# Kernel optimization log

Hardware: AMD Instinct MI355X
Metric: run time of the kernel (lower is better)

Reference implementation:

```python
import jax, jax.numpy as jnp
import numpy as np
from jax import lax

HEADS = 8
HEAD_C = 16  # attention_channels // heads = 128 // 8


def setup_inputs() -> dict:
    key = jax.random.key(0)
    ks = jax.random.split(key, 16)
    N, I, H, W = 8, 128, 36, 36
    R, C, A, O = 128, 128, 128, 128  # recurrent, common, attention, out channels
    s = lambda *sh: 0.05
    inp = {
        'x': jax.random.normal(ks[0], (N, I, H, W), jnp.float32),
        # input 1x1 conv (Accumulate of single Conv, bias init 0)
        'w_in': jax.random.normal(ks[1], (R, I), jnp.float32) * 0.05,
        'b_in': jnp.zeros((R,), jnp.float32),
        # 3x3 conv on cat([x, h]) -> common channels
        'w_conv': jax.random.normal(ks[2], (C, 2 * R, 3, 3), jnp.float32) * 0.05,
        'b_conv': jnp.zeros((C,), jnp.float32),
        # q/k/v 1x1 projections (no bias)
        'wq': jax.random.normal(ks[3], (A, C), jnp.float32) * 0.05,
        'wk': jax.random.normal(ks[4], (A, C), jnp.float32) * 0.05,
        'wv': jax.random.normal(ks[5], (A, C), jnp.float32) * 0.05,
        # gate 1x1 projections on cat([z, a]) (C + A inputs)
        'w_i': jax.random.normal(ks[6], (R, C + A), jnp.float32) * 0.05,
        'b_i': jnp.full((R,), -1.0, jnp.float32),  # init_input
        'w_f': jax.random.normal(ks[7], (R, C + A), jnp.float32) * 0.05,
        'b_f': jnp.full((R,), 1.0, jnp.float32),   # init_forget
        'w_g': jax.random.normal(ks[8], (R, C + A), jnp.float32) * 0.05,
        'b_g': jnp.zeros((R,), jnp.float32),
        'w_o': jax.random.normal(ks[9], (R, C + A), jnp.float32) * 0.05,
        'b_o': jnp.zeros((R,), jnp.float32),
        # output 1x1 conv
        'w_out': jax.random.normal(ks[10], (O, R), jnp.float32) * 0.05,
        'b_out': jnp.zeros((O,), jnp.float32),
    }
    return inp


def _conv1x1(w, x, b=None):
    y = jnp.einsum('oi,nihw->nohw', w, x)
    if b is not None:
        y = y + b[None, :, None, None]
    return y


def reference(x, w_in, b_in, w_conv, b_conv, wq, wk, wv,
              w_i, b_i, w_f, b_f, w_g, b_g, w_o, b_o, w_out, b_out):
    # first timestep: past is empty -> h = c = 0
    xt = jnp.tanh(_conv1x1(w_in, x, b_in))          # [N, R, H, W]
    h0 = jnp.zeros_like(xt)
    c0 = jnp.zeros_like(xt)
    xh = jnp.concatenate([xt, h0], axis=1)          # groups=1 -> plain concat
    z = lax.conv_general_dilated(xh, w_conv, (1, 1), 'SAME') + b_conv[None, :, None, None]
    N, C, H, W = z.shape
    HW = H * W
    q = _conv1x1(wq, z).reshape(N, HEADS, HEAD_C, HW)
    k = _conv1x1(wk, z).reshape(N, HEADS, HEAD_C, HW)
    v = _conv1x1(wv, z).reshape(N, HEADS, HEAD_C, HW)
    # spatial attention over H*W tokens per head
    w_attn = jax.nn.softmax(jnp.einsum('nhcq,nhcd->nhqd', q, k), axis=-1)  # [N,heads,HW,HW]
    a = jnp.einsum('nhcd,nhqd->nhcq', v, w_attn).reshape(N, -1, H, W)      # [N,A,H,W]
    za = jnp.concatenate([z, a], axis=1)
    i = jax.nn.sigmoid(_conv1x1(w_i, za, b_i))
    f = jax.nn.sigmoid(_conv1x1(w_f, za, b_f))
    g = jnp.tanh(_conv1x1(w_g, za, b_g))
    o = jax.nn.sigmoid(_conv1x1(w_o, za, b_o))
    c = f * c0 + i * g
    h = o * jnp.tanh(c)  # dropout p=0 -> identity
    return _conv1x1(w_out, h, b_out)
```

## Files before the change

### kernel.cpp

```cpp
#include <hip/hip_runtime.h>
#include <hip/hip_bf16.h>
#include <math.h>

typedef __hip_bfloat16 bf16;
typedef __attribute__((ext_vector_type(8))) short frag8;
typedef __attribute__((ext_vector_type(4))) float f32x4;
typedef __attribute__((ext_vector_type(16))) float f32x16;
typedef __attribute__((ext_vector_type(2))) unsigned int u32x2;
typedef __attribute__((ext_vector_type(4))) unsigned int u32x4;

#define HW  1296
#define CH  128
#define TT  1327104

__device__ __forceinline__ float b2f(bf16 v) { return __bfloat162float(v); }
__device__ __forceinline__ float bits2f(unsigned short u) {
    return __uint_as_float(((unsigned)u) << 16);
}
__device__ __forceinline__ float frcp(float x) { return __builtin_amdgcn_rcpf(x); }
__device__ __forceinline__ float fsigm(float x) { return frcp(1.0f + __expf(-x)); }
__device__ __forceinline__ float ftanh(float x) {
    float xc = fminf(15.0f, fmaxf(-15.0f, x));
    float e = __expf(2.0f * xc);
    return (e - 1.0f) * frcp(e + 1.0f);
}
__device__ __forceinline__ int packrh(float a, float b) {
    unsigned ua = __float_as_uint(a) + 0x8000u;
    unsigned ub = __float_as_uint(b) + 0x8000u;
    return (int)__builtin_amdgcn_perm(ub, ua, 0x07060302);
}
__device__ __forceinline__ int2 pack4(float a, float b, float c, float d) {
    int2 r; r.x = packrh(a, b); r.y = packrh(c, d); return r;
}
__device__ __forceinline__ unsigned cvtpk(float a, float b) {
    unsigned r;
    asm("v_cvt_pk_bf16_f32 %0, %1, %2" : "=v"(r) : "v"(a), "v"(b));
    return r;
}

__device__ __forceinline__ int detect_f32(const void* w) {
    const short4* p = (const short4*)w;
    short4 v = p[threadIdx.x & 63];
    int bad = 0;
    #pragma unroll
    for (int j = 0; j < 4; ++j) {
        float f = bits2f(((const unsigned short*)&v)[j]);
        if (!(fabsf(f) <= 100.0f)) bad = 1;
    }
    return __any(bad) ? 1 : 0;
}

__global__ __launch_bounds__(256) void k_prep(
    const void* w_in, const void* w_conv, const void* wq, const void* wk, const void* wv,
    const void* w_i, const void* w_g, const void* w_o, const void* w_out,
    const void* b_in, const void* b_conv, const void* b_i, const void* b_g,
    const void* b_o, const void* b_out,
    bf16* __restrict__ Wdst, float* __restrict__ Bdst)
{
    int idx = blockIdx.x * 256 + threadIdx.x;
    const int f = detect_f32(w_in);
    if (idx < 327680) {
        const void* src; int si;
        if (idx < 16384)       { src = w_in; si = idx; }
        else if (idx < 163840) { int j = idx - 16384; int tap = j >> 14, rem = j & 16383;
                                 int o = rem >> 7, r = rem & 127;
                                 src = w_conv; si = o * 2304 + r * 9 + tap; }
        else if (idx < 212992) { int j = idx - 163840; int o = j >> 7, i = j & 127;
                                 int ws_ = o >> 7;
                                 src = ws_ == 0 ? wq : ws_ == 1 ? wk : wv;
                                 si = (o & 127) * 128 + i; }
        else if (idx < 311296) { int j = idx - 212992; int g = j >> 15, rem = j & 32767;
                                 int o = rem >> 8, k = rem & 255;
                                 src = g == 0 ? w_i : g == 1 ? w_g : w_o; si = o * 256 + k; }
        else                   { int j = idx - 311296; int o = j >> 7, i = j & 127;
                                 src = w_out; si = o * 128 + i; }
        float v = f ? ((const float*)src)[si] : b2f(((const bf16*)src)[si]);
        if (idx >= 163840 && idx < 180224) v *= 1.4426950408889634f;
        Wdst[idx] = __float2bfloat16(v);
    } else if (idx < 327680 + 768) {
        int j = idx - 327680; int b = j >> 7, e = j & 127;
        const void* src = b == 0 ? b_in : b == 1 ? b_conv : b == 2 ? b_i
                        : b == 3 ? b_g : b == 4 ? b_o : b_out;
        Bdst[j] = f ? ((const float*)src)[e] : b2f(((const bf16*)src)[e]);
    }
}

__global__ __launch_bounds__(256) void k_inm(const void* __restrict__ x,
                                             const void* __restrict__ wraw,
                                             const bf16* __restrict__ Wm,
                                             const float* __restrict__ bias,
                                             bf16* __restrict__ XT) {
    __shared__ short Xl[32][132];
    const int tid = threadIdx.x, wave = tid >> 6, lane = tid & 63;
    const int quad = lane >> 4, l16 = lane & 15;
    const int n = blockIdx.x;
    const int pbase = blockIdx.y * 32;
    const int obase = blockIdx.z * 32 + (wave & 1) * 16;
    const int pstrip = (wave >> 1) * 16;
    const int f = detect_f32(wraw);

    frag8 WF[4];
    #pragma unroll
    for (int kc = 0; kc < 4; ++kc)
        WF[kc] = *(const frag8*)&Wm[(obase + l16) * CH + kc * 32 + quad * 8];

    #pragma unroll
    for (int rep = 0; rep < 4; ++rep) {
        int u = tid + rep * 256;
        int i = u >> 3;
        int p4 = (u & 7) * 4;
        int p = pbase + p4;
        short4 s = {0, 0, 0, 0};
        if (p < HW) {
            size_t gi = (size_t)n * CH * HW + (size_t)i * HW + p;
            if (f) {
                float4 fv = *(const float4*)((const float*)x + gi);
                int2 pk = pack4(fv.x, fv.y, fv.z, fv.w);
                s = *(short4*)&pk;
            } else {
                s = *(const short4*)((const bf16*)x + gi);
            }
        }
        Xl[p4 + 0][i] = s.x; Xl[p4 + 1][i] = s.y;
        Xl[p4 + 2][i] = s.z; Xl[p4 + 3][i] = s.w;
    }
    __syncthreads();

    const int pl = pstrip + l16;
    f32x4 acc = {0.f, 0.f, 0.f, 0.f};
    #pragma unroll
    for (int kc = 0; kc < 4; ++kc) {
        int k = kc * 32 + quad * 8;
        short4 b0 = *(const short4*)&Xl[pl][k];
        short4 b1 = *(const short4*)&Xl[pl][k + 4];
        frag8 bf = {b0.x, b0.y, b0.z, b0.w, b1.x, b1.y, b1.z, b1.w};
        acc = __builtin_amdgcn_mfma_f32_16x16x32_bf16(WF[kc], bf, acc, 0, 0, 0);
    }

    int p = pbase + pstrip + l16;
    if (p < HW) {
        int og = obase + quad * 4;
        int2 pk = pack4(ftanh(acc[0] + bias[og + 0]), ftanh(acc[1] + bias[og + 1]),
                        ftanh(acc[2] + bias[og + 2]), ftanh(acc[3] + bias[og + 3]));
        *(int2*)((short*)XT + ((size_t)n * HW + p) * CH + og) = pk;
    }
}

__global__ __launch_bounds__(512) void k_cq(
    const bf16* __restrict__ XT, const bf16* __restrict__ Wc,
    const float* __restrict__ bc, const bf16* __restrict__ Wqkv,
    bf16* __restrict__ Zb, bf16* __restrict__ Qb, bf16* __restrict__ Kb,
    bf16* __restrict__ Vb)
{
    __shared__ short Zl[32][136];
    const int tid = threadIdx.x, w = tid >> 6, lane = tid & 63;
    const int quad = lane >> 4, l16 = lane & 15;
    const int n = blockIdx.x;
    const int pbase = blockIdx.y * 32;
    const bf16* actn = XT + (size_t)n * HW * CH;

    const int obase = w * 16;
    const int p1 = pbase + l16, p2 = pbase + 16 + l16;
    const bool p1ok = p1 < HW, p2ok = p2 < HW;
    const int h1 = p1 / 36, w1 = p1 - h1 * 36;
    const int h2 = p2 / 36, w2 = p2 - h2 * 36;

    frag8 zf = {0, 0, 0, 0, 0, 0, 0, 0};
    f32x4 acc[2];
    acc[0] = (f32x4){0.f, 0.f, 0.f, 0.f};
    acc[1] = (f32x4){0.f, 0.f, 0.f, 0.f};

    frag8 A1[2][4], A2[2][4], WT[2][4];

    #define LOADTAP(TAP, BUF)                                                        \
    {                                                                                \
        const int dy = (TAP) / 3 - 1, dx = (TAP) - ((TAP) / 3) * 3 - 1;              \
        const bool ok1 = p1ok && (unsigned)(h1 + dy) < 36u && (unsigned)(w1 + dx) < 36u; \
        const bool ok2 = p2ok && (unsigned)(h2 + dy) < 36u && (unsigned)(w2 + dx) < 36u; \
        const int sh = dy * 36 + dx;                                                 \
        const bf16* a1 = actn + (size_t)(p1 + sh) * CH + quad * 8;                   \
        const bf16* a2 = actn + (size_t)(p2 + sh) * CH + quad * 8;                   \
        const bf16* wp = Wc + (TAP) * 16384 + (obase + l16) * CH + quad * 8;         \
        _Pragma("unroll")                                                            \
        for (int kc = 0; kc < 4; ++kc) {                                             \
            A1[BUF][kc] = ok1 ? *(const frag8*)&a1[kc * 32] : zf;                    \
            A2[BUF][kc] = ok2 ? *(const frag8*)&a2[kc * 32] : zf;                    \
            WT[BUF][kc] = *(const frag8*)&wp[kc * 32];                               \
        }                                                                            \
    }

    LOADTAP(0, 0);
    #pragma unroll
    for (int tap = 0; tap < 9; ++tap) {
        const int cur = tap & 1;
        if (tap < 8) LOADTAP(tap + 1, cur ^ 1);
        #pragma unroll
        for (int kc = 0; kc < 4; ++kc) {
            acc[0] = __builtin_amdgcn_mfma_f32_16x16x32_bf16(WT[cur][kc], A1[cur][kc], acc[0], 0, 0, 0);
            acc[1] = __builtin_amdgcn_mfma_f32_16x16x32_bf16(WT[cur][kc], A2[cur][kc], acc[1], 0, 0, 0);
        }
    }
    #undef LOADTAP

    const int og = obase + quad * 4;
    #pragma unroll
    for (int pt = 0; pt < 2; ++pt) {
        int p = pbase + pt * 16 + l16;
        int2 pk = pack4(acc[pt][0] + bc[og + 0], acc[pt][1] + bc[og + 1],
                        acc[pt][2] + bc[og + 2], acc[pt][3] + bc[og + 3]);
        *(int2*)&Zl[pt * 16 + l16][og] = pk;
        if (p < HW)
            *(int2*)((short*)Zb + ((size_t)n * HW + p) * CH + og) = pk;
    }
    __syncthreads();

    for (int ot = w; ot < 12; ot += 8) {
        const bool vt = (ot >= 8);
        const int ob = ot * 32;
        frag8 B1[4], B2[4], W0a[4], W1a[4];
        #pragma unroll
        for (int kc = 0; kc < 4; ++kc) {
            int ko = kc * 32 + quad * 8;
            B1[kc]  = *(const frag8*)&Zl[l16][ko];
            B2[kc]  = *(const frag8*)&Zl[16 + l16][ko];
            W0a[kc] = *(const frag8*)&Wqkv[(size_t)(ob + l16) * CH + ko];
            W1a[kc] = *(const frag8*)&Wqkv[(size_t)(ob + 16 + l16) * CH + ko];
        }

        f32x4 qacc[2][2];
        #pragma unroll
        for (int of = 0; of < 2; ++of) {
            qacc[of][0] = (f32x4){0.f, 0.f, 0.f, 0.f};
            qacc[of][1] = (f32x4){0.f, 0.f, 0.f, 0.f};
        }
        #pragma unroll
        for (int kc = 0; kc < 4; ++kc) {
            if (vt) {
                qacc[0][0] = __builtin_amdgcn_mfma_f32_16x16x32_bf16(B1[kc], W0a[kc], qacc[0][0], 0, 0, 0);
                qacc[0][1] = __builtin_amdgcn_mfma_f32_16x16x32_bf16(B2[kc], W0a[kc], qacc[0][1], 0, 0, 0);
                qacc[1][0] = __builtin_amdgcn_mfma_f32_16x16x32_bf16(B1[kc], W1a[kc], qacc[1][0], 0, 0, 0);
                qacc[1][1] = __builtin_amdgcn_mfma_f32_16x16x32_bf16(B2[kc], W1a[kc], qacc[1][1], 0, 0, 0);
            } else {
                qacc[0][0] = __builtin_amdgcn_mfma_f32_16x16x32_bf16(W0a[kc], B1[kc], qacc[0][0], 0, 0, 0);
                qacc[0][1] = __builtin_amdgcn_mfma_f32_16x16x32_bf16(W0a[kc], B2[kc], qacc[0][1], 0, 0, 0);
                qacc[1][0] = __builtin_amdgcn_mfma_f32_16x16x32_bf16(W1a[kc], B1[kc], qacc[1][0], 0, 0, 0);
                qacc[1][1] = __builtin_amdgcn_mfma_f32_16x16x32_bf16(W1a[kc], B2[kc], qacc[1][1], 0, 0, 0);
            }
        }

        if (vt) {
            #pragma unroll
            for (int of = 0; of < 2; ++of) {
                int ov = ob + of * 16 - 256 + l16;
                #pragma unroll
                for (int pt = 0; pt < 2; ++pt) {
                    int p4 = pbase + pt * 16 + quad * 4;
                    if (p4 >= HW) continue;
                    int2 pk = pack4(qacc[of][pt][0], qacc[of][pt][1], qacc[of][pt][2], qacc[of][pt][3]);
                    *(int2*)((short*)Vb + ((size_t)n * CH + ov) * HW + p4) = pk;
                }
            }
        } else {
            #pragma unroll
            for (int of = 0; of < 2; ++of) {
                int ogq = ob + of * 16 + quad * 4;
                int which = ogq >> 7, ol = ogq & 127;
                bf16* dst = which == 0 ? Qb : Kb;
                #pragma unroll
                for (int pt = 0; pt < 2; ++pt) {
                    int p = pbase + pt * 16 + l16;
                    if (p >= HW) continue;
                    size_t di = (((size_t)n * 8 + (ol >> 4)) * HW + p) * 16 + (ol & 15);
                    int2 pk = pack4(qacc[of][pt][0], qacc[of][pt][1], qacc[of][pt][2], qacc[of][pt][3]);
                    *(int2*)((short*)dst + di) = pk;
                }
            }
        }
    }
}

__global__ __launch_bounds__(256) void k_cell(
    const bf16* __restrict__ Zb, const bf16* __restrict__ Ab,
    const bf16* __restrict__ Wg, const float* __restrict__ bg,
    const bf16* __restrict__ Wo, const float* __restrict__ bo,
    void* __restrict__ out, const void* __restrict__ wraw)
{
    __shared__ short Hl[16][136];
    const int tid = threadIdx.x, w = tid >> 6, lane = tid & 63;
    const int quad = lane >> 4, l16 = lane & 15;
    const int n = blockIdx.x;
    const int pbase = blockIdx.y * 16;
    const int f32f = detect_f32(wraw);
    const bf16* zn = Zb + (size_t)n * HW * CH;
    const bf16* an = Ab + (size_t)n * HW * CH;

    const int obase = w * 32;
    const int p1 = pbase + l16;

    f32x4 acc[3][2];
    #pragma unroll
    for (int g = 0; g < 3; ++g) {
        acc[g][0] = (f32x4){0.f, 0.f, 0.f, 0.f};
        acc[g][1] = (f32x4){0.f, 0.f, 0.f, 0.f};
    }

    frag8 GB[2];
    frag8 GW[2][6];

    #define LOADG(KC, BUF)                                                           \
    {                                                                                \
        const bf16* src = ((KC) >= 4) ? an : zn;                                     \
        const int ko = ((KC) & 3) * 32 + quad * 8;                                   \
        GB[BUF] = *(const frag8*)&src[(size_t)p1 * CH + ko];                         \
        _Pragma("unroll")                                                            \
        for (int g = 0; g < 3; ++g) {                                                \
            _Pragma("unroll")                                                        \
            for (int of = 0; of < 2; ++of)                                           \
                GW[BUF][g * 2 + of] = *(const frag8*)&Wg[g * 32768 +                 \
                    (obase + of * 16 + l16) * 256 + (KC) * 32 + quad * 8];           \
        }                                                                            \
    }

    LOADG(0, 0);
    #pragma unroll
    for (int kc = 0; kc < 8; ++kc) {
        const int cur = kc & 1;
        if (kc < 7) LOADG(kc + 1, cur ^ 1);
        #pragma unroll
        for (int g = 0; g < 3; ++g) {
            #pragma unroll
            for (int of = 0; of < 2; ++of)
                acc[g][of] = __builtin_amdgcn_mfma_f32_16x16x32_bf16(
                    GW[cur][g * 2 + of], GB[cur], acc[g][of], 0, 0, 0);
        }
    }
    #undef LOADG

    #pragma unroll
    for (int of = 0; of < 2; ++of) {
        int og = obase + of * 16 + quad * 4;
        float hv[4];
        #pragma unroll
        for (int r = 0; r < 4; ++r) {
            int o = og + r;
            float iv = fsigm(acc[0][of][r] + bg[o]);
            float gv = ftanh(acc[1][of][r] + bg[128 + o]);
            float ov = fsigm(acc[2][of][r] + bg[256 + o]);
            hv[r] = ov * ftanh(iv * gv);
        }
        *(int2*)&Hl[l16][og] = pack4(hv[0], hv[1], hv[2], hv[3]);
    }

    frag8 OW[2][4];
    #pragma unroll
    for (int of = 0; of < 2; ++of)
        #pragma unroll
        for (int kc = 0; kc < 4; ++kc)
            OW[of][kc] = *(const frag8*)&Wo[(size_t)(obase + of * 16 + l16) * CH
                                            + kc * 32 + quad * 8];
    __syncthreads();

    f32x4 oc[2];
    oc[0] = (f32x4){0.f, 0.f, 0.f, 0.f};
    oc[1] = (f32x4){0.f, 0.f, 0.f, 0.f};
    #pragma unroll
    for (int kc = 0; kc < 4; ++kc) {
        int k = kc * 32 + quad * 8;
        short4 h0 = *(const short4*)&Hl[l16][k];
        short4 h1 = *(const short4*)&Hl[l16][k + 4];
        frag8 af = {h0.x, h0.y, h0.z, h0.w, h1.x, h1.y, h1.z, h1.w};
        #pragma unroll
        for (int of = 0; of < 2; ++of)
            oc[of] = __builtin_amdgcn_mfma_f32_16x16x32_bf16(af, OW[of][kc], oc[of], 0, 0, 0);
    }
    int p4 = pbase + quad * 4;
    #pragma unroll
    for (int of = 0; of < 2; ++of) {
        int o = obase + of * 16 + l16;
        float bv = bo[o];
        size_t di = ((size_t)n * CH + o) * HW + p4;
        if (f32f) {
            float4 fv = {oc[of][0] + bv, oc[of][1] + bv, oc[of][2] + bv, oc[of][3] + bv};
            *(float4*)&((float*)out)[di] = fv;
        } else {
            int2 pk = pack4(oc[of][0] + bv, oc[of][1] + bv, oc[of][2] + bv, oc[of][3] + bv);
            *(int2*)&((short*)out)[di] = pk;
        }
    }
}

__global__ __launch_bounds__(512) void k_attn(const bf16* __restrict__ Qg,
                                              const bf16* __restrict__ Kg,
                                              const bf16* __restrict__ Vcf,
                                              bf16* __restrict__ A) {
    __shared__ float Lc[4][9][64];

    const int tid = threadIdx.x;
    const int w = tid >> 6, lane = tid & 63;
    const int l32 = lane & 31, hi = lane >> 5;
    const int qw = w & 3, dq = w >> 2;
    const int n = blockIdx.x;
    const int head = blockIdx.z;
    const int qb = blockIdx.y * 128 + qw * 32;
    const int qtok = qb + l32;

    const short* Qh = (const short*)Qg + ((size_t)(n * 8 + head)) * HW * 16;
    const short* Kh = (const short*)Kg + ((size_t)(n * 8 + head)) * HW * 16;
    const short* Vh = (const short*)Vcf + ((size_t)n * CH + head * 16) * HW;

    frag8 qf = {0, 0, 0, 0, 0, 0, 0, 0};
    if (qtok < HW) qf = *(const frag8*)&Qh[(size_t)qtok * 16 + hi * 8];

    const short one = (short)0x3F80;
    const frag8 vones = {one, one, one, one, one, one, one, one};
    const frag8 vzero = {0, 0, 0, 0, 0, 0, 0, 0};
    const frag8 vfill = (l32 == 16) ? vones : vzero;
    const bool vload = l32 < 16;
    const short* Vrow = Vh + (size_t)(vload ? l32 : 0) * HW;

    const f32x16 zero16 = {};
    f32x16 Oacc = {};

    auto KLD = [&](int dd) -> frag8 {
        return *(const frag8*)&Kh[(size_t)(dd + l32) * 16 + hi * 8];
    };
    auto VLD = [&](int dd) -> frag8 {
        return vload ? *(const frag8*)&Vrow[dd + hi * 8] : vfill;
    };

    const int c0 = dq ? 20 : 0;
    frag8 kf  = KLD(c0 * 32);
    frag8 kf2 = KLD(c0 * 32 + 32);
    frag8 va  = VLD(c0 * 32);
    frag8 vb  = VLD(c0 * 32 + 16);
    f32x16 S = __builtin_amdgcn_mfma_f32_32x32x16_bf16(kf, qf, zero16, 0, 0, 0);

    for (int it = 0; it < 20; ++it) {
        const int d0 = (c0 + it) * 32;
        frag8 kn  = KLD(d0 + 64);
        frag8 van = VLD(d0 + 32);
        frag8 vbn = VLD(d0 + 48);
        f32x16 Sn = __builtin_amdgcn_mfma_f32_32x32x16_bf16(kf2, qf, zero16, 0, 0, 0);

        float p[16];
        #pragma unroll
        for (int r = 0; r < 16; ++r) p[r] = __builtin_amdgcn_exp2f(S[r]);

        #pragma unroll
        for (int hh = 0; hh < 2; ++hh) {
            unsigned P0 = cvtpk(p[hh * 8 + 0], p[hh * 8 + 1]);
            unsigned P1 = cvtpk(p[hh * 8 + 2], p[hh * 8 + 3]);
            unsigned P2 = cvtpk(p[hh * 8 + 4], p[hh * 8 + 5]);
            unsigned P3 = cvtpk(p[hh * 8 + 6], p[hh * 8 + 7]);
            u32x2 s02 = __builtin_amdgcn_permlane32_swap(P0, P2, false, false);
            u32x2 s13 = __builtin_amdgcn_permlane32_swap(P1, P3, false, false);
            u32x4 bw = {s02[0], s13[0], s02[1], s13[1]};
            frag8 pf = __builtin_bit_cast(frag8, bw);
            Oacc = __builtin_amdgcn_mfma_f32_32x32x16_bf16(hh ? vb : va, pf, Oacc, 0, 0, 0);
        }
        kf2 = kn; va = van; vb = vbn; S = Sn;
    }

    if (dq) {
        float p[8];
        #pragma unroll
        for (int r = 0; r < 8; ++r) p[r] = __builtin_amdgcn_exp2f(S[r]);
        unsigned P0 = cvtpk(p[0], p[1]);
        unsigned P1 = cvtpk(p[2], p[3]);
        unsigned P2 = cvtpk(p[4], p[5]);
        unsigned P3 = cvtpk(p[6], p[7]);
        u32x2 s02 = __builtin_amdgcn_permlane32_swap(P0, P2, false, false);
        u32x2 s13 = __builtin_amdgcn_permlane32_swap(P1, P3, false, false);
        u32x4 bw = {s02[0], s13[0], s02[1], s13[1]};
        frag8 pf = __builtin_bit_cast(frag8, bw);
        Oacc = __builtin_amdgcn_mfma_f32_32x32x16_bf16(va, pf, Oacc, 0, 0, 0);
        #pragma unroll
        for (int r = 0; r < 8; ++r) Lc[qw][r][lane] = Oacc[r];
        Lc[qw][8][lane] = Oacc[8];
    }
    __syncthreads();
    if (dq == 0) {
        #pragma unroll
        for (int r = 0; r < 8; ++r) Oacc[r] += Lc[qw][r][lane];
        float lsum = Oacc[8] + Lc[qw][8][lane];
        u32x2 lb = __builtin_amdgcn_permlane32_swap(__float_as_uint(lsum),
                                                    __float_as_uint(lsum), false, false);
        float inv = frcp(__uint_as_float(lb[0]));
        if (qtok < HW) {
            short* An = (short*)A + ((size_t)n * HW + qtok) * CH + head * 16;
            int2 pk0 = pack4(Oacc[0] * inv, Oacc[1] * inv, Oacc[2] * inv, Oacc[3] * inv);
            int2 pk1 = pack4(Oacc[4] * inv, Oacc[5] * inv, Oacc[6] * inv, Oacc[7] * inv);
            *(int2*)&An[hi * 4] = pk0;
            *(int2*)&An[8 + hi * 4] = pk1;
        }
    }
}

extern "C" void kernel_launch(void* const* d_in, const int* in_sizes, int n_in,
                              void* d_out, int out_size, void* d_ws, size_t ws_size,
                              hipStream_t stream) {
    char* ws = (char*)d_ws;
    bf16*  Wst  = (bf16*)(ws + 256);
    float* Bst  = (float*)(ws + 655616);
    bf16*  XT   = (bf16*)(ws + 1048576);
    bf16*  Zb   = XT + TT;
    bf16*  Qb   = Zb + TT;
    bf16*  Kb   = Qb + TT;
    bf16*  Vb   = Kb + TT;
    bf16*  Ab   = Vb + TT;

    k_prep<<<1284, 256, 0, stream>>>(d_in[1], d_in[3], d_in[5], d_in[6], d_in[7],
                                     d_in[8], d_in[12], d_in[14], d_in[16],
                                     d_in[2], d_in[4], d_in[9], d_in[13], d_in[15], d_in[17],
                                     Wst, Bst);
    k_inm<<<dim3(8, 41, 4), 256, 0, stream>>>(d_in[0], d_in[1], Wst, Bst, XT);
    k_cq<<<dim3(8, 41), 512, 0, stream>>>(XT, Wst + 16384, Bst + 128, Wst + 163840,
                                          Zb, Qb, Kb, Vb);
    k_attn<<<dim3(8, 11, 8), 512, 0, stream>>>(Qb, Kb, Vb, Ab);
    k_cell<<<dim3(8, 81), 256, 0, stream>>>(Zb, Ab, Wst + 212992, Bst + 256,
                                            Wst + 311296, Bst + 640, d_out, d_in[1]);
}
```

Before: 199.6 us.

## Split 3x3 conv taps across wave groups with LDS reduction in k_cq

```diff
diff --git a/kernel.cpp b/kernel.cpp
--- a/kernel.cpp
+++ b/kernel.cpp
@@ -153,64 +153,83 @@
     bf16* __restrict__ Vb)
 {
     __shared__ short Zl[32][136];
+    __shared__ float Rd[4][4][4][64];
     const int tid = threadIdx.x, w = tid >> 6, lane = tid & 63;
     const int quad = lane >> 4, l16 = lane & 15;
     const int n = blockIdx.x;
     const int pbase = blockIdx.y * 32;
     const bf16* actn = XT + (size_t)n * HW * CH;
 
-    const int obase = w * 16;
+    const int o4 = w & 3, tg = w >> 2;
+    const int obase = o4 * 32;
     const int p1 = pbase + l16, p2 = pbase + 16 + l16;
     const bool p1ok = p1 < HW, p2ok = p2 < HW;
     const int h1 = p1 / 36, w1 = p1 - h1 * 36;
     const int h2 = p2 / 36, w2 = p2 - h2 * 36;
 
     frag8 zf = {0, 0, 0, 0, 0, 0, 0, 0};
-    f32x4 acc[2];
-    acc[0] = (f32x4){0.f, 0.f, 0.f, 0.f};
-    acc[1] = (f32x4){0.f, 0.f, 0.f, 0.f};
-
-    frag8 A1[2][4], A2[2][4], WT[2][4];
-
-    #define LOADTAP(TAP, BUF)                                                        \
-    {                                                                                \
-        const int dy = (TAP) / 3 - 1, dx = (TAP) - ((TAP) / 3) * 3 - 1;              \
-        const bool ok1 = p1ok && (unsigned)(h1 + dy) < 36u && (unsigned)(w1 + dx) < 36u; \
-        const bool ok2 = p2ok && (unsigned)(h2 + dy) < 36u && (unsigned)(w2 + dx) < 36u; \
-        const int sh = dy * 36 + dx;                                                 \
-        const bf16* a1 = actn + (size_t)(p1 + sh) * CH + quad * 8;                   \
-        const bf16* a2 = actn + (size_t)(p2 + sh) * CH + quad * 8;                   \
-        const bf16* wp = Wc + (TAP) * 16384 + (obase + l16) * CH + quad * 8;         \
-        _Pragma("unroll")                                                            \
-        for (int kc = 0; kc < 4; ++kc) {                                             \
-            A1[BUF][kc] = ok1 ? *(const frag8*)&a1[kc * 32] : zf;                    \
-            A2[BUF][kc] = ok2 ? *(const frag8*)&a2[kc * 32] : zf;                    \
-            WT[BUF][kc] = *(const frag8*)&wp[kc * 32];                               \
-        }                                                                            \
-    }
-
-    LOADTAP(0, 0);
-    #pragma unroll
-    for (int tap = 0; tap < 9; ++tap) {
-        const int cur = tap & 1;
-        if (tap < 8) LOADTAP(tap + 1, cur ^ 1);
+    f32x4 acc[2][2];
+    #pragma unroll
+    for (int of = 0; of < 2; ++of) {
+        acc[of][0] = (f32x4){0.f, 0.f, 0.f, 0.f};
+        acc[of][1] = (f32x4){0.f, 0.f, 0.f, 0.f};
+    }
+
+    const int tap0 = tg ? 5 : 0, tap1 = tg ? 9 : 5;
+    for (int tap = tap0; tap < tap1; ++tap) {
+        const int dy = tap / 3 - 1, dx = tap - (tap / 3) * 3 - 1;
+        const bool ok1 = p1ok && (unsigned)(h1 + dy) < 36u && (unsigned)(w1 + dx) < 36u;
+        const bool ok2 = p2ok && (unsigned)(h2 + dy) < 36u && (unsigned)(w2 + dx) < 36u;
+        const int sh = dy * 36 + dx;
+        const bf16* a1 = actn + (size_t)(p1 + sh) * CH + quad * 8;
+        const bf16* a2 = actn + (size_t)(p2 + sh) * CH + quad * 8;
+        const bf16* wp0 = Wc + tap * 16384 + (obase + l16) * CH + quad * 8;
+        const bf16* wp1 = Wc + tap * 16384 + (obase + 16 + l16) * CH + quad * 8;
+        frag8 A1[4], A2[4], W0[4], W1[4];
         #pragma unroll
         for (int kc = 0; kc < 4; ++kc) {
-            acc[0] = __builtin_amdgcn_mfma_f32_16x16x32_bf16(WT[cur][kc], A1[cur][kc], acc[0], 0, 0, 0);
-            acc[1] = __builtin_amdgcn_mfma_f32_16x16x32_bf16(WT[cur][kc], A2[cur][kc], acc[1], 0, 0, 0);
-        }
-    }
-    #undef LOADTAP
-
-    const int og = obase + quad * 4;
-    #pragma unroll
-    for (int pt = 0; pt < 2; ++pt) {
-        int p = pbase + pt * 16 + l16;
-        int2 pk = pack4(acc[pt][0] + bc[og + 0], acc[pt][1] + bc[og + 1],
-                        acc[pt][2] + bc[og + 2], acc[pt][3] + bc[og + 3]);
-        *(int2*)&Zl[pt * 16 + l16][og] = pk;
-        if (p < HW)
-            *(int2*)((short*)Zb + ((size_t)n * HW + p) * CH + og) = pk;
+            A1[kc] = ok1 ? *(const frag8*)&a1[kc * 32] : zf;
+            A2[kc] = ok2 ? *(const frag8*)&a2[kc * 32] : zf;
+            W0[kc] = *(const frag8*)&wp0[kc * 32];
+            W1[kc] = *(const frag8*)&wp1[kc * 32];
+        }
+        #pragma unroll
+        for (int kc = 0; kc < 4; ++kc) {
+            acc[0][0] = __builtin_amdgcn_mfma_f32_16x16x32_bf16(W0[kc], A1[kc], acc[0][0], 0, 0, 0);
+            acc[0][1] = __builtin_amdgcn_mfma_f32_16x16x32_bf16(W0[kc], A2[kc], acc[0][1], 0, 0, 0);
+            acc[1][0] = __builtin_amdgcn_mfma_f32_16x16x32_bf16(W1[kc], A1[kc], acc[1][0], 0, 0, 0);
+            acc[1][1] = __builtin_amdgcn_mfma_f32_16x16x32_bf16(W1[kc], A2[kc], acc[1][1], 0, 0, 0);
+        }
+    }
+
+    if (tg == 1) {
+        #pragma unroll
+        for (int of = 0; of < 2; ++of)
+            #pragma unroll
+            for (int pt = 0; pt < 2; ++pt)
+                #pragma unroll
+                for (int r = 0; r < 4; ++r)
+                    Rd[o4][of * 2 + pt][r][lane] = acc[of][pt][r];
+    }
+    __syncthreads();
+    if (tg == 0) {
+        #pragma unroll
+        for (int of = 0; of < 2; ++of) {
+            #pragma unroll
+            for (int pt = 0; pt < 2; ++pt) {
+                #pragma unroll
+                for (int r = 0; r < 4; ++r)
+                    acc[of][pt][r] += Rd[o4][of * 2 + pt][r][lane];
+                int og = obase + of * 16 + quad * 4;
+                int pl = pt * 16 + l16;
+                int p = pbase + pl;
+                int2 pk = pack4(acc[of][pt][0] + bc[og + 0], acc[of][pt][1] + bc[og + 1],
+                                acc[of][pt][2] + bc[og + 2], acc[of][pt][3] + bc[og + 3]);
+                *(int2*)&Zl[pl][og] = pk;
+                if (p < HW)
+                    *(int2*)((short*)Zb + ((size_t)n * HW + p) * CH + og) = pk;
+            }
+        }
     }
     __syncthreads();
 
```

Result: faster. 185.0 us (-7.3%).
